# Performance work log

Measured on AMD Instinct MI355X. Metric: run time of the kernel, lower is better.

The kernel has to match this reference:

```python
import jax, jax.numpy as jnp
import numpy as np

CONSTRAINT_WEIGHT = 0.5
FOCAL_GAMMA = 2.0
EPS = 1e-8

B, G, C = 65536, 9, 9
BLK = 3  # int(sqrt(G))


def setup_inputs() -> dict:
    key = jax.random.key(0)
    k1, k2, k3 = jax.random.split(key, 3)
    logits = jax.random.normal(k1, (B, G, G, C), dtype=jnp.float32)
    targets = jax.random.randint(k2, (B, G, G), 0, 10, dtype=jnp.int64)
    puzzles = jax.random.randint(k3, (B, G, G), 0, 10, dtype=jnp.int64)
    return {"logits": logits, "targets": targets, "puzzles": puzzles}


def _sudoku_loss(logits, targets, puzzles):
    b, g, _, c = logits.shape
    mask = (puzzles == 0).astype(logits.dtype)            # [B,G,G]
    tgt = jnp.clip(targets - 1, 0, c - 1)                 # [B,G,G]

    log_probs = jax.nn.log_softmax(logits, axis=-1)       # [B,G,G,C]
    probs = jnp.exp(log_probs)

    # --- focal CE over masked (empty) cells ---
    lp_t = jnp.take_along_axis(log_probs, tgt[..., None], axis=-1)[..., 0]  # [B,G,G]
    pt = jnp.exp(lp_t)
    ce = -lp_t
    focal = (1.0 - pt) ** FOCAL_GAMMA * ce
    msum = mask.sum()
    ce_loss = (focal * mask).sum() / (msum + EPS)

    # --- constraint loss ---
    masked_probs = probs * mask[..., None]                # [B,G,G,C]
    row_sums = masked_probs.sum(axis=2)                   # [B,G,C]
    row_loss = jnp.mean((row_sums - 1.0) ** 2)
    col_sums = masked_probs.sum(axis=1)                   # [B,G,C]
    col_loss = jnp.mean((col_sums - 1.0) ** 2)
    # boxes: [B, br, r, bc, c_in, C] -> sum over the 3x3 cells of each box
    box = masked_probs.reshape(b, BLK, BLK, BLK, BLK, c)
    box_sums = box.transpose(0, 1, 3, 2, 4, 5).reshape(b, BLK * BLK, BLK * BLK, c).sum(axis=2)
    box_loss = jnp.mean((box_sums - 1.0) ** 2)

    entropy = -(probs * log_probs).sum(axis=-1)           # [B,G,G]
    entropy_loss = 0.1 * ((entropy * mask).sum() / (msum + EPS))

    top2, _ = jax.lax.top_k(probs, 2)                     # [B,G,G,2]
    gap = top2[..., 0] - top2[..., 1]
    uniqueness_loss = 0.1 * jnp.mean(jax.nn.relu(1.0 - gap))

    constraint_loss = (row_loss + col_loss + box_loss + entropy_loss + uniqueness_loss) * 0.2
    return ce_loss + CONSTRAINT_WEIGHT * constraint_loss


def reference(logits, targets, puzzles):
    return _sudoku_loss(logits, targets, puzzles)
```

## Files before the change

kernel.cpp:

```cpp
#include <hip/hip_runtime.h>

#define THREADS 256
#define WORKERS 243

__global__ __launch_bounds__(THREADS) void sudoku_main(
    const float* __restrict__ logits,
    const int*   __restrict__ targets,
    const int*   __restrict__ puzzles,
    float* __restrict__ acc,
    int B, int numTriples)
{
  __shared__ float sprob[3 * 81 * 9];
  __shared__ float sred[4][5];

  const int tid    = threadIdx.x;
  const bool worker = tid < WORKERS;
  const int lp   = tid / 81;
  const int cell = tid % 81;

  const int ut   = lp;
  const int uidx = cell / 9;
  const int uch  = cell % 9;
  int ucell[9];
#pragma unroll
  for (int j = 0; j < 9; ++j) {
    if (ut == 0)      ucell[j] = uidx * 9 + j;
    else if (ut == 1) ucell[j] = j * 9 + uidx;
    else              ucell[j] = (uidx / 3) * 27 + (uidx % 3) * 3
                                  + (j / 3) * 9 + (j % 3);
  }

  float a_focal = 0.f, a_ent = 0.f, a_msk = 0.f, a_uniq = 0.f, a_sq = 0.f;

  for (int t = blockIdx.x; t < numTriples; t += gridDim.x) {
    const int p = t * 3 + lp;
    const bool valid = worker && (p < B);
    if (worker) {
      if (valid) {
        const size_t cidx = (size_t)p * 81 + cell;
        const float* Lp = logits + cidx * 9;
        float l[9];
#pragma unroll
        for (int i = 0; i < 9; ++i) l[i] = Lp[i];
        float m = l[0];
#pragma unroll
        for (int i = 1; i < 9; ++i) m = fmaxf(m, l[i]);
        float e[9], s = 0.f, lsum = 0.f, e1 = -1.f, e2 = -1.f;
#pragma unroll
        for (int i = 0; i < 9; ++i) {
          float x  = l[i] - m;
          float ei = __expf(x);
          e[i] = ei;
          s += ei;
          lsum += ei * x;
          if (ei > e1) { e2 = e1; e1 = ei; }
          else if (ei > e2) { e2 = ei; }
        }
        float inv_s = 1.f / s;
        float logs  = __logf(s);

        int tg = targets[cidx] - 1;
        tg = tg < 0 ? 0 : (tg > 8 ? 8 : tg);
        float lpt   = (l[tg] - m) - logs;
        float pt    = e[tg] * inv_s;
        float om    = 1.f - pt;
        float focal = om * om * (-lpt);

        float ent = logs - lsum * inv_s;
        float gap = (e1 - e2) * inv_s;
        float uq  = fmaxf(0.f, 1.f - gap);

        float mk = (puzzles[cidx] == 0) ? 1.f : 0.f;
        a_focal += focal * mk;
        a_ent   += ent * mk;
        a_msk   += mk;
        a_uniq  += uq;

        float pm = inv_s * mk;
#pragma unroll
        for (int i = 0; i < 9; ++i) sprob[tid * 9 + i] = e[i] * pm;
      } else {
#pragma unroll
        for (int i = 0; i < 9; ++i) sprob[tid * 9 + i] = 0.f;
      }
    }
    __syncthreads();
    if (worker) {
#pragma unroll
      for (int k = 0; k < 3; ++k) {
        if (t * 3 + k < B) {
          float s = 0.f;
#pragma unroll
          for (int j = 0; j < 9; ++j)
            s += sprob[(k * 81 + ucell[j]) * 9 + uch];
          float d = s - 1.f;
          a_sq += d * d;
        }
      }
    }
    __syncthreads();
  }

#pragma unroll
  for (int off = 32; off > 0; off >>= 1) {
    a_focal += __shfl_down(a_focal, off);
    a_ent   += __shfl_down(a_ent,   off);
    a_msk   += __shfl_down(a_msk,   off);
    a_uniq  += __shfl_down(a_uniq,  off);
    a_sq    += __shfl_down(a_sq,    off);
  }
  const int wave = tid >> 6;
  if ((tid & 63) == 0) {
    sred[wave][0] = a_focal; sred[wave][1] = a_ent; sred[wave][2] = a_msk;
    sred[wave][3] = a_uniq;  sred[wave][4] = a_sq;
  }
  __syncthreads();
  if (tid < 5) {
    float v = sred[0][tid] + sred[1][tid] + sred[2][tid] + sred[3][tid];
    atomicAdd(&acc[tid], v);
  }
}

__global__ void sudoku_finalize(const float* __restrict__ acc,
                                float* __restrict__ out, float invBG)
{
  float focal = acc[0], ent = acc[1], msum = acc[2], uniq = acc[3], sq = acc[4];
  float inv_m = 1.f / (msum + 1e-8f);
  float ce    = focal * inv_m;
  float entl  = 0.1f * ent * inv_m;
  float uql   = 0.1f * uniq * invBG;
  float rcb   = sq * invBG;
  float constraint = (rcb + entl + uql) * 0.2f;
  out[0] = ce + 0.5f * constraint;
}

extern "C" void kernel_launch(void* const* d_in, const int* in_sizes, int n_in,
                              void* d_out, int out_size, void* d_ws, size_t ws_size,
                              hipStream_t stream)
{
  (void)n_in; (void)out_size; (void)ws_size;
  const float* logits  = (const float*)d_in[0];
  const int*   targets = (const int*)d_in[1];
  const int*   puzzles = (const int*)d_in[2];
  float* out = (float*)d_out;
  float* acc = (float*)d_ws;

  const int B = in_sizes[0] / 729;
  const int numTriples = (B + 2) / 3;

  hipMemsetAsync(acc, 0, 5 * sizeof(float), stream);

  int grid = numTriples < 2048 ? numTriples : 2048;
  sudoku_main<<<grid, THREADS, 0, stream>>>(logits, targets, puzzles, acc, B, numTriples);

  const float invBG = 1.f / ((float)B * 81.f);
  sudoku_finalize<<<1, 1, 0, stream>>>(acc, out, invBG);
}
```

Baseline: 68.97 us.

## Stage logits through LDS with coalesced float4 loads, process 4 puzzles per block

Each block now copies a contiguous chunk of 4 puzzles' logits into shared memory with coalesced float4 loads. It then computes the per-cell softmax from LDS and reuses the same buffer for the row, column and box sums. Before this, each thread read 9 strided floats straight from global memory. The change targets uncoalesced global reads and idle threads, at the cost of an extra barrier per group and possible LDS bank conflicts on stride-9 accesses.

```diff
diff --git a/kernel.cpp b/kernel.cpp
--- a/kernel.cpp
+++ b/kernel.cpp
@@ -1,47 +1,54 @@
 #include <hip/hip_runtime.h>
 
 #define THREADS 256
-#define WORKERS 243
+#define PB 4
 
 __global__ __launch_bounds__(THREADS) void sudoku_main(
     const float* __restrict__ logits,
     const int*   __restrict__ targets,
     const int*   __restrict__ puzzles,
     float* __restrict__ acc,
-    int B, int numTriples)
+    int B)
 {
-  __shared__ float sprob[3 * 81 * 9];
+  __shared__ float lds[PB * 729];
   __shared__ float sred[4][5];
 
-  const int tid    = threadIdx.x;
-  const bool worker = tid < WORKERS;
-  const int lp   = tid / 81;
-  const int cell = tid % 81;
-
-  const int ut   = lp;
-  const int uidx = cell / 9;
-  const int uch  = cell % 9;
-  int ucell[9];
-#pragma unroll
-  for (int j = 0; j < 9; ++j) {
-    if (ut == 0)      ucell[j] = uidx * 9 + j;
-    else if (ut == 1) ucell[j] = j * 9 + uidx;
-    else              ucell[j] = (uidx / 3) * 27 + (uidx % 3) * 3
-                                  + (j / 3) * 9 + (j % 3);
-  }
+  const int tid = threadIdx.x;
+  const int numGroups = (B + PB - 1) / PB;
 
   float a_focal = 0.f, a_ent = 0.f, a_msk = 0.f, a_uniq = 0.f, a_sq = 0.f;
 
-  for (int t = blockIdx.x; t < numTriples; t += gridDim.x) {
-    const int p = t * 3 + lp;
-    const bool valid = worker && (p < B);
-    if (worker) {
-      if (valid) {
-        const size_t cidx = (size_t)p * 81 + cell;
-        const float* Lp = logits + cidx * 9;
+  for (int g = blockIdx.x; g < numGroups; g += gridDim.x) {
+    const int grp = min(PB, B - g * PB);
+    const int nf  = grp * 729;
+
+    {
+      const float4* src4 = (const float4*)(logits + (size_t)g * (PB * 729));
+      float4* dst4 = (float4*)lds;
+      const int nf4 = nf >> 2;
+#pragma unroll
+      for (int r = 0; r < (PB * 729 / 4 + THREADS - 1) / THREADS; ++r) {
+        int idx = tid + r * THREADS;
+        if (idx < nf4) dst4[idx] = src4[idx];
+      }
+      int remBase = nf4 << 2;
+      if (tid < (nf - remBase))
+        lds[remBase + tid] = logits[(size_t)g * (PB * 729) + remBase + tid];
+    }
+    __syncthreads();
+
+#pragma unroll
+    for (int r = 0; r < (PB * 81 + THREADS - 1) / THREADS; ++r) {
+      int c = tid + r * THREADS;
+      if (c < grp * 81) {
+        const size_t cidx = (size_t)g * (PB * 81) + c;
+        int tg = targets[cidx] - 1;
+        int pz = puzzles[cidx];
+        tg = tg < 0 ? 0 : (tg > 8 ? 8 : tg);
+
         float l[9];
 #pragma unroll
-        for (int i = 0; i < 9; ++i) l[i] = Lp[i];
+        for (int i = 0; i < 9; ++i) l[i] = lds[c * 9 + i];
         float m = l[0];
 #pragma unroll
         for (int i = 1; i < 9; ++i) m = fmaxf(m, l[i]);
@@ -59,8 +66,6 @@
         float inv_s = 1.f / s;
         float logs  = __logf(s);
 
-        int tg = targets[cidx] - 1;
-        tg = tg < 0 ? 0 : (tg > 8 ? 8 : tg);
         float lpt   = (l[tg] - m) - logs;
         float pt    = e[tg] * inv_s;
         float om    = 1.f - pt;
@@ -70,7 +75,7 @@
         float gap = (e1 - e2) * inv_s;
         float uq  = fmaxf(0.f, 1.f - gap);
 
-        float mk = (puzzles[cidx] == 0) ? 1.f : 0.f;
+        float mk = (pz == 0) ? 1.f : 0.f;
         a_focal += focal * mk;
         a_ent   += ent * mk;
         a_msk   += mk;
@@ -78,24 +83,34 @@
 
         float pm = inv_s * mk;
 #pragma unroll
-        for (int i = 0; i < 9; ++i) sprob[tid * 9 + i] = e[i] * pm;
-      } else {
-#pragma unroll
-        for (int i = 0; i < 9; ++i) sprob[tid * 9 + i] = 0.f;
+        for (int i = 0; i < 9; ++i) lds[c * 9 + i] = e[i] * pm;
       }
     }
     __syncthreads();
-    if (worker) {
+
 #pragma unroll
-      for (int k = 0; k < 3; ++k) {
-        if (t * 3 + k < B) {
-          float s = 0.f;
+    for (int r = 0; r < (PB * 243 + THREADS - 1) / THREADS; ++r) {
+      int s = tid + r * THREADS;
+      if (s < grp * 243) {
+        int lp = s / 243;
+        int u  = s - lp * 243;
+        int ut = u / 81;
+        int v  = u - ut * 81;
+        int uidx = v / 9;
+        int uch  = v - uidx * 9;
+        int base = lp * 729;
+        float ssum = 0.f;
 #pragma unroll
-          for (int j = 0; j < 9; ++j)
-            s += sprob[(k * 81 + ucell[j]) * 9 + uch];
-          float d = s - 1.f;
-          a_sq += d * d;
+        for (int j = 0; j < 9; ++j) {
+          int cell;
+          if (ut == 0)      cell = uidx * 9 + j;
+          else if (ut == 1) cell = j * 9 + uidx;
+          else              cell = (uidx / 3) * 27 + (uidx % 3) * 3
+                                   + (j / 3) * 9 + (j % 3);
+          ssum += lds[base + cell * 9 + uch];
         }
+        float d = ssum - 1.f;
+        a_sq += d * d;
       }
     }
     __syncthreads();
@@ -146,12 +161,12 @@
   float* acc = (float*)d_ws;
 
   const int B = in_sizes[0] / 729;
-  const int numTriples = (B + 2) / 3;
+  const int numGroups = (B + PB - 1) / PB;
 
   hipMemsetAsync(acc, 0, 5 * sizeof(float), stream);
 
-  int grid = numTriples < 2048 ? numTriples : 2048;
-  sudoku_main<<<grid, THREADS, 0, stream>>>(logits, targets, puzzles, acc, B, numTriples);
+  int grid = numGroups < 2048 ? numGroups : 2048;
+  sudoku_main<<<grid, THREADS, 0, stream>>>(logits, targets, puzzles, acc, B);
 
   const float invBG = 1.f / ((float)B * 81.f);
   sudoku_finalize<<<1, 1, 0, stream>>>(acc, out, invBG);
```

Result: slower. 78.68 us (+14.1%).
